# Kernel tuning notes

Hardware: AMD Instinct MI355X
Metric: run time of the kernel (lower is better)

## Reference

```python
import jax, jax.numpy as jnp
import numpy as np

E, D, H, K = 8, 1024, 4096, 2  # num_experts, input/output dim, hidden dim, top-k
B, S = 2, 2048


def setup_inputs() -> dict:
    key = jax.random.key(0)
    ks = jax.random.split(key, 5)
    s = 0.02
    return {
        "x": jax.random.normal(ks[0], (B, S, D), dtype=jnp.float32),
        "router_w": jax.random.normal(ks[1], (D, E), dtype=jnp.float32) * s,
        "router_b": jnp.zeros((E,), jnp.float32),
        "w1": jax.random.normal(ks[2], (E, D, H), dtype=jnp.float32) * s,
        "b1": jnp.zeros((E, H), jnp.float32),
        "w2": jax.random.normal(ks[3], (E, H, D), dtype=jnp.float32) * s,
        "b2": jnp.zeros((E, D), jnp.float32),
        "gamma": jnp.ones((E, D), jnp.float32),
        "beta": jnp.zeros((E, D), jnp.float32),
    }


def _layernorm(y, g, b, eps=1e-5):
    mu = y.mean(-1, keepdims=True)
    var = ((y - mu) ** 2).mean(-1, keepdims=True)
    return (y - mu) * jax.lax.rsqrt(var + eps) * g + b


def reference(x, router_w, router_b, w1, b1, w2, b2, gamma, beta):
    # Router
    router_logits = x @ router_w + router_b            # [B,S,E]
    probs = jax.nn.softmax(router_logits, axis=-1)
    topk_p, topk_i = jax.lax.top_k(probs, K)           # [B,S,K]
    topk_p = topk_p / topk_p.sum(-1, keepdims=True)

    # All experts over all tokens (equivalent to the masked dense loop,
    # since every expert op is per-token). Dropout = identity (eval).
    h = jax.nn.gelu(jnp.einsum('bsd,edh->ebsh', x, w1) + b1[:, None, None, :],
                    approximate=False)                  # [E,B,S,H]
    y = jnp.einsum('ebsh,ehd->ebsd', h, w2) + b2[:, None, None, :]
    eo = _layernorm(y + x[None], gamma[:, None, None, :], beta[:, None, None, :])  # [E,B,S,D]

    # Combine top-k experts per token
    eo = jnp.moveaxis(eo, 0, 2)                         # [B,S,E,D]
    gathered = jnp.take_along_axis(eo, topk_i[..., None], axis=2)  # [B,S,K,D]
    output = (gathered * topk_p[..., None]).sum(axis=2)            # [B,S,D]
    return output, router_logits
```

## Files before the change

### kernel.cpp

```cpp
#include <hip/hip_runtime.h>
#include <math.h>

#define NE 8
#define DD 1024
#define HH 4096
#define TT 4096
#define RR 8192

typedef __attribute__((ext_vector_type(8))) short short8;
typedef __attribute__((ext_vector_type(4))) float f32x4;

__device__ __forceinline__ unsigned short f2bf(float f) {
    unsigned int u = __float_as_uint(f);
    u += 0x7fffu + ((u >> 16) & 1u);
    return (unsigned short)(u >> 16);
}

__device__ __forceinline__ float gelu_fast(float v) {
    float z = fabsf(v) * 0.70710678f;
    float t = __fdividef(1.0f, fmaf(0.3275911f, z, 1.0f));
    float p = fmaf(1.061405429f, t, -1.453152027f);
    p = fmaf(p, t, 1.421413741f);
    p = fmaf(p, t, -0.284496736f);
    p = fmaf(p, t, 0.254829592f);
    p = p * t;
    float erf = fmaf(-p, __expf(-z * z), 1.0f);
    return 0.5f * v * (1.0f + copysignf(erf, v));
}

__device__ __forceinline__ void async_copy16(void* lds, const void* g) {
    auto* lp = reinterpret_cast<__attribute__((address_space(3))) unsigned int*>(
        (unsigned int)(unsigned long long)(lds));
    auto* gp = reinterpret_cast<const __attribute__((address_space(1))) unsigned int*>(
        (unsigned long long)(g));
    __builtin_amdgcn_global_load_lds(gp, lp, 16, 0, 0);
}


__global__ void cvtx_kernel(const float* __restrict__ x, unsigned short* __restrict__ xb) {
    size_t i = (size_t)(blockIdx.x * 256 + threadIdx.x) * 4;
    float4 v = *(const float4*)&x[i];
    unsigned int lo = (unsigned int)f2bf(v.x) | ((unsigned int)f2bf(v.y) << 16);
    unsigned int hi = (unsigned int)f2bf(v.z) | ((unsigned int)f2bf(v.w) << 16);
    *(uint2*)&xb[i] = make_uint2(lo, hi);
}

__global__ __launch_bounds__(256) void transpose_swz_kernel(const float* __restrict__ src,
        unsigned short* __restrict__ dst, int K, int N) {
    const int e = blockIdx.z;
    src += (size_t)e * K * N;
    dst += (size_t)e * K * N;
    const int c0 = blockIdx.x * 64;
    const int r0 = blockIdx.y * 64;
    __shared__ unsigned short t[64][65];
    const int tid = threadIdx.x;
    const int rc4 = (tid & 15) * 4, rr = tid >> 4;
    #pragma unroll
    for (int i = 0; i < 4; i++) {
        int r = rr + i * 16;
        float4 v = *(const float4*)&src[(size_t)(r0 + r) * N + c0 + rc4];
        t[r][rc4]     = f2bf(v.x);
        t[r][rc4 + 1] = f2bf(v.y);
        t[r][rc4 + 2] = f2bf(v.z);
        t[r][rc4 + 3] = f2bf(v.w);
    }
    __syncthreads();
    const int n_local = tid & 63;
    const int n = c0 + n_local;
    const int nt = n >> 7, row = n & 127;
    const int Kdiv32 = K >> 5;
    #pragma unroll
    for (int it = 0; it < 2; it++) {
        int dg = (tid >> 6) + 4 * it;
        int kb = 2 * blockIdx.y + (dg >> 2);
        int q = dg & 3;
        unsigned short tmp[8];
        #pragma unroll
        for (int i = 0; i < 8; i++) tmp[i] = t[dg * 8 + i][n_local];
        size_t idx = ((((size_t)nt * Kdiv32 + kb) * 4 + q) * 128 + row) * 8;
        *(uint4*)&dst[idx] = *(uint4*)&tmp[0];
    }
}

__global__ void router_kernel(const float* __restrict__ x, const float* __restrict__ rw,
                              const float* __restrict__ rb, float* __restrict__ logits_out,
                              int* __restrict__ topk_e, float* __restrict__ topk_p,
                              int* __restrict__ counts) {
    const int t = blockIdx.x;
    const int tid = threadIdx.x;
    float4 xv = *(const float4*)&x[(size_t)t * DD + tid * 4];
    const float* rwp = rw + (size_t)(tid * 4) * NE;
    float acc[NE];
    #pragma unroll
    for (int e = 0; e < NE; e++) acc[e] = 0.f;
    float xs[4] = {xv.x, xv.y, xv.z, xv.w};
    #pragma unroll
    for (int i = 0; i < 4; i++) {
        #pragma unroll
        for (int e = 0; e < NE; e++) acc[e] += xs[i] * rwp[i * NE + e];
    }
    #pragma unroll
    for (int e = 0; e < NE; e++) {
        float v = acc[e];
        for (int off = 32; off > 0; off >>= 1) v += __shfl_down(v, off);
        acc[e] = v;
    }
    __shared__ float part[4][NE];
    if ((tid & 63) == 0) {
        #pragma unroll
        for (int e = 0; e < NE; e++) part[tid >> 6][e] = acc[e];
    }
    __syncthreads();
    if (tid == 0) {
        float lg[NE];
        #pragma unroll
        for (int e = 0; e < NE; e++)
            lg[e] = part[0][e] + part[1][e] + part[2][e] + part[3][e] + rb[e];
        #pragma unroll
        for (int e = 0; e < NE; e++) logits_out[(size_t)t * NE + e] = lg[e];
        float m = lg[0];
        #pragma unroll
        for (int e = 1; e < NE; e++) m = fmaxf(m, lg[e]);
        float pr[NE];
        #pragma unroll
        for (int e = 0; e < NE; e++) pr[e] = __expf(lg[e] - m);
        int i0 = 0;
        #pragma unroll
        for (int e = 1; e < NE; e++) if (pr[e] > pr[i0]) i0 = e;
        int i1 = (i0 == 0) ? 1 : 0;
        #pragma unroll
        for (int e = 0; e < NE; e++) if (e != i0 && pr[e] > pr[i1]) i1 = e;
        float p0 = pr[i0], p1 = pr[i1];
        float inv = 1.f / (p0 + p1);
        topk_e[t * 2] = i0;  topk_e[t * 2 + 1] = i1;
        topk_p[t * 2] = p0 * inv;  topk_p[t * 2 + 1] = p1 * inv;
        atomicAdd(&counts[i0], 1);
        atomicAdd(&counts[i1], 1);
    }
}

__global__ void prefix_kernel(const int* __restrict__ counts, int* __restrict__ offs,
                              int* __restrict__ cursor) {
    if (threadIdx.x == 0) {
        int a = 0;
        for (int e = 0; e < NE; e++) { offs[e] = a; cursor[e] = a; a += counts[e]; }
        offs[NE] = a;
    }
}

__global__ void scatter_kernel(const int* __restrict__ topk_e, int* __restrict__ cursor,
                               int* __restrict__ row_token, int* __restrict__ slot_of) {
    int i = blockIdx.x * 256 + threadIdx.x;
    int e = topk_e[i];
    int pos = atomicAdd(&cursor[e], 1);
    row_token[pos] = i >> 1;
    slot_of[i] = pos;
}

__device__ __forceinline__ void mfma_step(const unsigned short* Ab, const unsigned short* Bb,
        int wr, int wc, int m16, int q, f32x4 (&acc)[4][4]) {
    short8 af[4], bfr[4];
    #pragma unroll
    for (int i = 0; i < 4; i++) af[i] = *(const short8*)&Ab[q * 1024 + (wr + i * 16 + m16) * 8];
    #pragma unroll
    for (int j = 0; j < 4; j++) bfr[j] = *(const short8*)&Bb[q * 1024 + (wc + j * 16 + m16) * 8];
    #pragma unroll
    for (int i = 0; i < 4; i++)
        #pragma unroll
        for (int j = 0; j < 4; j++)
            acc[i][j] = __builtin_amdgcn_mfma_f32_16x16x32_bf16(af[i], bfr[j], acc[i][j], 0, 0, 0);
}

template <int NK>
__device__ __forceinline__ void kloop_3s(
        const unsigned short* ag0, const unsigned short* ag1, const unsigned short* bg,
        unsigned short* As, unsigned short* Bs,
        int wv, int lane, int wr, int wc, int m16, int q, f32x4 (&acc)[4][4]) {
    unsigned short* alA = As + wv * 1024 + lane * 8;
    unsigned short* blB = Bs + wv * 1024 + lane * 8;

    #pragma unroll
    for (int p = 0; p < 2; ++p) {
        async_copy16(alA + p * 4096, ag0); async_copy16(alA + p * 4096 + 512, ag1);
        async_copy16(blB + p * 4096, bg);  async_copy16(blB + p * 4096 + 512, bg + 512);
        ag0 += 32; ag1 += 32; bg += 4096;
    }

    int cOff = 0;
    int sOff = 2 * 4096;
    #pragma unroll 1
    for (int t = 0; t < NK - 2; ++t) {
        async_copy16(alA + sOff, ag0); async_copy16(alA + sOff + 512, ag1);
        async_copy16(blB + sOff, bg);  async_copy16(blB + sOff + 512, bg + 512);
        ag0 += 32; ag1 += 32; bg += 4096;
        asm volatile("s_waitcnt vmcnt(8)" ::: "memory");
        __builtin_amdgcn_s_barrier();
        mfma_step(As + cOff, Bs + cOff, wr, wc, m16, q, acc);
        __builtin_amdgcn_s_barrier();
        sOff = cOff;
        cOff += 4096; if (cOff == 3 * 4096) cOff = 0;
    }
    asm volatile("s_waitcnt vmcnt(4)" ::: "memory");
    __builtin_amdgcn_s_barrier();
    mfma_step(As + cOff, Bs + cOff, wr, wc, m16, q, acc);
    cOff += 4096; if (cOff == 3 * 4096) cOff = 0;
    asm volatile("s_waitcnt vmcnt(0)" ::: "memory");
    __builtin_amdgcn_s_barrier();
    mfma_step(As + cOff, Bs + cOff, wr, wc, m16, q, acc);
}

__global__ __launch_bounds__(256) void gemm1_kernel(
        const unsigned short* __restrict__ xb, const unsigned short* __restrict__ w1s,
        const float* __restrict__ b1, const int* __restrict__ offs,
        const int* __restrict__ row_token, unsigned short* __restrict__ hbuf) {
    const int bid = blockIdx.x;
    const int xcd = bid & 7;
    const int mem = (bid >> 3) & 7;
    const int g   = (bid >> 6) * 8 + xcd;
    const int nth = g & 3;
    const int rt  = (g >> 2) & 31;
    const int e   = g >> 7;
    const int nt  = nth * 8 + mem;

    const int r0 = offs[e];
    const int ne = offs[e + 1] - r0;
    if (rt * 128 >= ne) return;

    __shared__ __align__(16) unsigned short As[3][4096];
    __shared__ __align__(16) unsigned short Bs[3][4096];

    const int tid = threadIdx.x;
    const int lane = tid & 63;
    const int wv = tid >> 6;
    const int wr = (wv >> 1) * 64, wc = (wv & 1) * 64;
    const int m16 = lane & 15, q = lane >> 4;

    int ra = rt * 128 + lane;       ra = ra < ne ? ra : ne - 1;
    int rb = rt * 128 + 64 + lane;  rb = rb < ne ? rb : ne - 1;
    const unsigned short* ag0 = xb + (size_t)row_token[r0 + ra] * DD + wv * 8;
    const unsigned short* ag1 = xb + (size_t)row_token[r0 + rb] * DD + wv * 8;

    const unsigned short* bg = w1s + (size_t)e * HH * DD + (size_t)nt * (DD >> 5) * 4096
                               + wv * 1024 + lane * 8;

    f32x4 acc[4][4];
    f32x4 zero = {0.f, 0.f, 0.f, 0.f};
    #pragma unroll
    for (int i = 0; i < 4; i++)
        #pragma unroll
        for (int j = 0; j < 4; j++) acc[i][j] = zero;

    kloop_3s<DD / 32>(ag0, ag1, bg, &As[0][0], &Bs[0][0], wv, lane, wr, wc, m16, q, acc);

    const int n0 = nt * 128;
    float b1v[4];
    #pragma unroll
    for (int j = 0; j < 4; j++) b1v[j] = b1[(size_t)e * HH + n0 + wc + j * 16 + m16];
    #pragma unroll
    for (int i = 0; i < 4; i++) {
        #pragma unroll
        for (int rg = 0; rg < 4; rg++) {
            int rr = rt * 128 + wr + i * 16 + q * 4 + rg;
            if (rr < ne) {
                unsigned short* hrow = hbuf + (size_t)(r0 + rr) * HH;
                #pragma unroll
                for (int j = 0; j < 4; j++) {
                    int col = n0 + wc + j * 16 + m16;
                    float v = acc[i][j][rg] + b1v[j];
                    hrow[col] = f2bf(gelu_fast(v));
                }
            }
        }
    }
}

__global__ __launch_bounds__(256) void gemm2_kernel(
        const unsigned short* __restrict__ hbuf, const unsigned short* __restrict__ w2s,
        const float* __restrict__ b2, const float* __restrict__ x,
        const int* __restrict__ offs, const int* __restrict__ row_token,
        float* __restrict__ yp) {
    const int bid = blockIdx.x;
    const int xcd = bid & 7;
    const int nt  = (bid >> 3) & 7;
    const int g   = (bid >> 6) * 8 + xcd;
    const int rt  = g & 31;
    const int e   = g >> 5;

    const int r0 = offs[e];
    const int ne = offs[e + 1] - r0;
    if (rt * 128 >= ne) return;

    __shared__ __align__(16) unsigned short As[3][4096];
    __shared__ __align__(16) unsigned short Bs[3][4096];

    const int tid = threadIdx.x;
    const int lane = tid & 63;
    const int wv = tid >> 6;
    const int wr = (wv >> 1) * 64, wc = (wv & 1) * 64;
    const int m16 = lane & 15, q = lane >> 4;

    int ra = rt * 128 + lane;       ra = ra < ne ? ra : ne - 1;
    int rb = rt * 128 + 64 + lane;  rb = rb < ne ? rb : ne - 1;
    const unsigned short* ag0 = hbuf + (size_t)(r0 + ra) * HH + wv * 8;
    const unsigned short* ag1 = hbuf + (size_t)(r0 + rb) * HH + wv * 8;

    const unsigned short* bg = w2s + (size_t)e * DD * HH + (size_t)nt * (HH >> 5) * 4096
                               + wv * 1024 + lane * 8;

    f32x4 acc[4][4];
    f32x4 zero = {0.f, 0.f, 0.f, 0.f};
    #pragma unroll
    for (int i = 0; i < 4; i++)
        #pragma unroll
        for (int j = 0; j < 4; j++) acc[i][j] = zero;

    kloop_3s<HH / 32>(ag0, ag1, bg, &As[0][0], &Bs[0][0], wv, lane, wr, wc, m16, q, acc);

    const int n0 = nt * 128;
    float b2v[4];
    #pragma unroll
    for (int j = 0; j < 4; j++) b2v[j] = b2[(size_t)e * DD + n0 + wc + j * 16 + m16];
    #pragma unroll
    for (int i = 0; i < 4; i++) {
        #pragma unroll
        for (int rg = 0; rg < 4; rg++) {
            int rr = rt * 128 + wr + i * 16 + q * 4 + rg;
            if (rr < ne) {
                float* yrow = yp + (size_t)(r0 + rr) * DD;
                int tok = row_token[r0 + rr];
                const float* xrow = x + (size_t)tok * DD;
                #pragma unroll
                for (int j = 0; j < 4; j++) {
                    int col = n0 + wc + j * 16 + m16;
                    yrow[col] = acc[i][j][rg] + b2v[j] + xrow[col];
                }
            }
        }
    }
}

__global__ void ln_combine_kernel(const float* __restrict__ yp,
                                  const int* __restrict__ slot_of,
                                  const int* __restrict__ topk_e, const float* __restrict__ topk_p,
                                  const float* __restrict__ gamma, const float* __restrict__ beta,
                                  float* __restrict__ out) {
    const int t = blockIdx.x;
    const int tid = threadIdx.x;
    __shared__ float ps[8];
    float4 o = {0.f, 0.f, 0.f, 0.f};
    #pragma unroll
    for (int k = 0; k < 2; k++) {
        int row = slot_of[t * 2 + k];
        int e = topk_e[t * 2 + k];
        float p = topk_p[t * 2 + k];
        float4 v = *(const float4*)&yp[(size_t)row * DD + tid * 4];
        float s = v.x + v.y + v.z + v.w;
        float sq = v.x * v.x + v.y * v.y + v.z * v.z + v.w * v.w;
        for (int off = 32; off > 0; off >>= 1) {
            s += __shfl_down(s, off);
            sq += __shfl_down(sq, off);
        }
        if ((tid & 63) == 0) { ps[tid >> 6] = s; ps[4 + (tid >> 6)] = sq; }
        __syncthreads();
        float fs = ps[0] + ps[1] + ps[2] + ps[3];
        float fq = ps[4] + ps[5] + ps[6] + ps[7];
        float mu = fs * (1.0f / DD);
        float var = fq * (1.0f / DD) - mu * mu;
        float rsig = rsqrtf(var + 1e-5f);
        float4 g = *(const float4*)&gamma[(size_t)e * DD + tid * 4];
        float4 bb = *(const float4*)&beta[(size_t)e * DD + tid * 4];
        o.x += p * ((v.x - mu) * rsig * g.x + bb.x);
        o.y += p * ((v.y - mu) * rsig * g.y + bb.y);
        o.z += p * ((v.z - mu) * rsig * g.z + bb.z);
        o.w += p * ((v.w - mu) * rsig * g.w + bb.w);
        __syncthreads();
    }
    *(float4*)&out[(size_t)t * DD + tid * 4] = o;
}

extern "C" void kernel_launch(void* const* d_in, const int* in_sizes, int n_in,
                              void* d_out, int out_size, void* d_ws, size_t ws_size,
                              hipStream_t stream) {
    const float* x     = (const float*)d_in[0];
    const float* rw    = (const float*)d_in[1];
    const float* rb    = (const float*)d_in[2];
    const float* w1    = (const float*)d_in[3];
    const float* b1    = (const float*)d_in[4];
    const float* w2    = (const float*)d_in[5];
    const float* b2    = (const float*)d_in[6];
    const float* gamma = (const float*)d_in[7];
    const float* beta  = (const float*)d_in[8];

    float* out    = (float*)d_out;
    float* logits = out + (size_t)TT * DD;

    char* w = (char*)d_ws;
    int*   counts    = (int*)(w + 0);
    int*   offs      = (int*)(w + 64);
    int*   cursor    = (int*)(w + 128);
    int*   topk_e    = (int*)(w + 4096);
    float* topk_p    = (float*)(w + 36864);
    int*   row_token = (int*)(w + 69632);
    int*   slot_of   = (int*)(w + 102400);
    unsigned short* xb   = (unsigned short*)(w + (size_t)1 * 1048576);
    unsigned short* w1s  = (unsigned short*)(w + (size_t)9 * 1048576);
    unsigned short* w2s  = (unsigned short*)(w + (size_t)73 * 1048576);
    unsigned short* hbuf = (unsigned short*)(w + (size_t)137 * 1048576);
    float*          yp   = (float*)(w + (size_t)1 * 1048576);

    hipMemsetAsync(w, 0, 1024, stream);

    transpose_swz_kernel<<<dim3(HH / 64, DD / 64, NE), 256, 0, stream>>>(w1, w1s, DD, HH);
    transpose_swz_kernel<<<dim3(DD / 64, HH / 64, NE), 256, 0, stream>>>(w2, w2s, HH, DD);
    cvtx_kernel<<<4096, 256, 0, stream>>>(x, xb);
    router_kernel<<<TT, 256, 0, stream>>>(x, rw, rb, logits, topk_e, topk_p, counts);
    prefix_kernel<<<1, 64, 0, stream>>>(counts, offs, cursor);
    scatter_kernel<<<RR / 256, 256, 0, stream>>>(topk_e, cursor, row_token, slot_of);
    gemm1_kernel<<<32 * 32 * NE, 256, 0, stream>>>(xb, w1s, b1, offs, row_token, hbuf);
    gemm2_kernel<<<8 * 32 * NE, 256, 0, stream>>>(hbuf, w2s, b2, x, offs, row_token, yp);
    ln_combine_kernel<<<TT, 256, 0, stream>>>(yp, slot_of, topk_e, topk_p, gamma, beta, out);
}
```

Baseline: 765.1 us.

## Compact expert tile list and split-K gemm2 into two partial buffers

```diff
diff --git a/kernel.cpp b/kernel.cpp
--- a/kernel.cpp
+++ b/kernel.cpp
@@ -140,11 +140,19 @@
 }
 
 __global__ void prefix_kernel(const int* __restrict__ counts, int* __restrict__ offs,
-                              int* __restrict__ cursor) {
+                              int* __restrict__ cursor, int* __restrict__ ntiles,
+                              int* __restrict__ tiles) {
     if (threadIdx.x == 0) {
         int a = 0;
         for (int e = 0; e < NE; e++) { offs[e] = a; cursor[e] = a; a += counts[e]; }
         offs[NE] = a;
+        int tc = 0;
+        for (int e = 0; e < NE; e++) {
+            int ne = offs[e + 1] - offs[e];
+            int nt = (ne + 127) >> 7;
+            for (int r = 0; r < nt; r++) tiles[tc++] = (e << 6) | r;
+        }
+        ntiles[0] = tc;
     }
 }
 
@@ -212,19 +220,17 @@
 __global__ __launch_bounds__(256) void gemm1_kernel(
         const unsigned short* __restrict__ xb, const unsigned short* __restrict__ w1s,
         const float* __restrict__ b1, const int* __restrict__ offs,
-        const int* __restrict__ row_token, unsigned short* __restrict__ hbuf) {
+        const int* __restrict__ row_token, const int* __restrict__ ntiles,
+        const int* __restrict__ tiles, unsigned short* __restrict__ hbuf) {
     const int bid = blockIdx.x;
-    const int xcd = bid & 7;
-    const int mem = (bid >> 3) & 7;
-    const int g   = (bid >> 6) * 8 + xcd;
-    const int nth = g & 3;
-    const int rt  = (g >> 2) & 31;
-    const int e   = g >> 7;
-    const int nt  = nth * 8 + mem;
+    const int t = bid >> 5;
+    const int nt = bid & 31;
+    if (t >= ntiles[0]) return;
+    const int pk = tiles[t];
+    const int e = pk >> 6, rt = pk & 63;
 
     const int r0 = offs[e];
     const int ne = offs[e + 1] - r0;
-    if (rt * 128 >= ne) return;
 
     __shared__ __align__(16) unsigned short As[3][4096];
     __shared__ __align__(16) unsigned short Bs[3][4096];
@@ -278,17 +284,21 @@
         const unsigned short* __restrict__ hbuf, const unsigned short* __restrict__ w2s,
         const float* __restrict__ b2, const float* __restrict__ x,
         const int* __restrict__ offs, const int* __restrict__ row_token,
-        float* __restrict__ yp) {
+        const int* __restrict__ ntiles, const int* __restrict__ tiles,
+        float* __restrict__ yp0, float* __restrict__ yp1) {
     const int bid = blockIdx.x;
-    const int xcd = bid & 7;
-    const int nt  = (bid >> 3) & 7;
-    const int g   = (bid >> 6) * 8 + xcd;
-    const int rt  = g & 31;
-    const int e   = g >> 5;
+    const int nt = (bid >> 3) & 7;
+    const int w = (bid >> 6) * 8 + (bid & 7);
+    const int t = w >> 1;
+    const int chunk = w & 1;
+    if (t >= ntiles[0]) return;
+    const int pk = tiles[t];
+    const int e = pk >> 6, rt = pk & 63;
 
     const int r0 = offs[e];
     const int ne = offs[e + 1] - r0;
-    if (rt * 128 >= ne) return;
+    const int kbase = chunk * (HH / 2);
+    float* ybuf = chunk ? yp1 : yp0;
 
     __shared__ __align__(16) unsigned short As[3][4096];
     __shared__ __align__(16) unsigned short Bs[3][4096];
@@ -301,11 +311,11 @@
 
     int ra = rt * 128 + lane;       ra = ra < ne ? ra : ne - 1;
     int rb = rt * 128 + 64 + lane;  rb = rb < ne ? rb : ne - 1;
-    const unsigned short* ag0 = hbuf + (size_t)(r0 + ra) * HH + wv * 8;
-    const unsigned short* ag1 = hbuf + (size_t)(r0 + rb) * HH + wv * 8;
+    const unsigned short* ag0 = hbuf + (size_t)(r0 + ra) * HH + kbase + wv * 8;
+    const unsigned short* ag1 = hbuf + (size_t)(r0 + rb) * HH + kbase + wv * 8;
 
     const unsigned short* bg = w2s + (size_t)e * DD * HH + (size_t)nt * (HH >> 5) * 4096
-                               + wv * 1024 + lane * 8;
+                               + (size_t)(kbase >> 5) * 4096 + wv * 1024 + lane * 8;
 
     f32x4 acc[4][4];
     f32x4 zero = {0.f, 0.f, 0.f, 0.f};
@@ -314,32 +324,42 @@
         #pragma unroll
         for (int j = 0; j < 4; j++) acc[i][j] = zero;
 
-    kloop_3s<HH / 32>(ag0, ag1, bg, &As[0][0], &Bs[0][0], wv, lane, wr, wc, m16, q, acc);
+    kloop_3s<(HH / 2) / 32>(ag0, ag1, bg, &As[0][0], &Bs[0][0], wv, lane, wr, wc, m16, q, acc);
 
     const int n0 = nt * 128;
-    float b2v[4];
-    #pragma unroll
-    for (int j = 0; j < 4; j++) b2v[j] = b2[(size_t)e * DD + n0 + wc + j * 16 + m16];
+    float b2v[4] = {0.f, 0.f, 0.f, 0.f};
+    if (chunk == 0) {
+        #pragma unroll
+        for (int j = 0; j < 4; j++) b2v[j] = b2[(size_t)e * DD + n0 + wc + j * 16 + m16];
+    }
     #pragma unroll
     for (int i = 0; i < 4; i++) {
         #pragma unroll
         for (int rg = 0; rg < 4; rg++) {
             int rr = rt * 128 + wr + i * 16 + q * 4 + rg;
             if (rr < ne) {
-                float* yrow = yp + (size_t)(r0 + rr) * DD;
-                int tok = row_token[r0 + rr];
-                const float* xrow = x + (size_t)tok * DD;
-                #pragma unroll
-                for (int j = 0; j < 4; j++) {
-                    int col = n0 + wc + j * 16 + m16;
-                    yrow[col] = acc[i][j][rg] + b2v[j] + xrow[col];
+                float* yrow = ybuf + (size_t)(r0 + rr) * DD;
+                if (chunk == 0) {
+                    int tok = row_token[r0 + rr];
+                    const float* xrow = x + (size_t)tok * DD;
+                    #pragma unroll
+                    for (int j = 0; j < 4; j++) {
+                        int col = n0 + wc + j * 16 + m16;
+                        yrow[col] = acc[i][j][rg] + b2v[j] + xrow[col];
+                    }
+                } else {
+                    #pragma unroll
+                    for (int j = 0; j < 4; j++) {
+                        int col = n0 + wc + j * 16 + m16;
+                        yrow[col] = acc[i][j][rg];
+                    }
                 }
             }
         }
     }
 }
 
-__global__ void ln_combine_kernel(const float* __restrict__ yp,
+__global__ void ln_combine_kernel(const float* __restrict__ yp0, const float* __restrict__ yp1,
                                   const int* __restrict__ slot_of,
                                   const int* __restrict__ topk_e, const float* __restrict__ topk_p,
                                   const float* __restrict__ gamma, const float* __restrict__ beta,
@@ -353,7 +373,9 @@
         int row = slot_of[t * 2 + k];
         int e = topk_e[t * 2 + k];
         float p = topk_p[t * 2 + k];
-        float4 v = *(const float4*)&yp[(size_t)row * DD + tid * 4];
+        float4 v0 = *(const float4*)&yp0[(size_t)row * DD + tid * 4];
+        float4 v1 = *(const float4*)&yp1[(size_t)row * DD + tid * 4];
+        float4 v = {v0.x + v1.x, v0.y + v1.y, v0.z + v1.z, v0.w + v1.w};
         float s = v.x + v.y + v.z + v.w;
         float sq = v.x * v.x + v.y * v.y + v.z * v.z + v.w * v.w;
         for (int off = 32; off > 0; off >>= 1) {
@@ -398,6 +420,8 @@
     int*   counts    = (int*)(w + 0);
     int*   offs      = (int*)(w + 64);
     int*   cursor    = (int*)(w + 128);
+    int*   ntiles    = (int*)(w + 192);
+    int*   tiles     = (int*)(w + 256);
     int*   topk_e    = (int*)(w + 4096);
     float* topk_p    = (float*)(w + 36864);
     int*   row_token = (int*)(w + 69632);
@@ -406,7 +430,8 @@
     unsigned short* w1s  = (unsigned short*)(w + (size_t)9 * 1048576);
     unsigned short* w2s  = (unsigned short*)(w + (size_t)73 * 1048576);
     unsigned short* hbuf = (unsigned short*)(w + (size_t)137 * 1048576);
-    float*          yp   = (float*)(w + (size_t)1 * 1048576);
+    float*          yp0  = (float*)(w + (size_t)1 * 1048576);
+    float*          yp1  = (float*)(w + (size_t)33 * 1048576);
 
     hipMemsetAsync(w, 0, 1024, stream);
 
@@ -414,9 +439,9 @@
     transpose_swz_kernel<<<dim3(DD / 64, HH / 64, NE), 256, 0, stream>>>(w2, w2s, HH, DD);
     cvtx_kernel<<<4096, 256, 0, stream>>>(x, xb);
     router_kernel<<<TT, 256, 0, stream>>>(x, rw, rb, logits, topk_e, topk_p, counts);
-    prefix_kernel<<<1, 64, 0, stream>>>(counts, offs, cursor);
+    prefix_kernel<<<1, 64, 0, stream>>>(counts, offs, cursor, ntiles, tiles);
     scatter_kernel<<<RR / 256, 256, 0, stream>>>(topk_e, cursor, row_token, slot_of);
-    gemm1_kernel<<<32 * 32 * NE, 256, 0, stream>>>(xb, w1s, b1, offs, row_token, hbuf);
-    gemm2_kernel<<<8 * 32 * NE, 256, 0, stream>>>(hbuf, w2s, b2, x, offs, row_token, yp);
-    ln_combine_kernel<<<TT, 256, 0, stream>>>(yp, slot_of, topk_e, topk_p, gamma, beta, out);
-}
+    gemm1_kernel<<<72 * 32, 256, 0, stream>>>(xb, w1s, b1, offs, row_token, ntiles, tiles, hbuf);
+    gemm2_kernel<<<18 * 64, 256, 0, stream>>>(hbuf, w2s, b2, x, offs, row_token, ntiles, tiles, yp0, yp1);
+    ln_combine_kernel<<<TT, 256, 0, stream>>>(yp0, yp1, slot_of, topk_e, topk_p, gamma, beta, out);
+}
```

Measured after the change: 742.1 us. 1.03x faster.
